# Kernel optimization log

Measured on AMD Instinct MI355X. Metric: run time of the kernel, lower is better.

The kernel has to match this reference:

```python
import jax, jax.numpy as jnp
import numpy as np

SCALING_FACTOR = 1.8
K = 10
ALPHA = 0.15
EPS = 1e-12


def setup_inputs() -> dict:
    key = jax.random.key(0)
    k1, k2, k3, k4 = jax.random.split(key, 4)
    N, E, IN, OUT = 100000, 3200000, 512, 256
    x = jax.random.normal(k1, (N, IN), dtype=jnp.float32)
    edge_index = jax.random.randint(k2, (2, E), 0, N, dtype=jnp.int64)
    W1 = jax.random.normal(k3, (OUT, IN), dtype=jnp.float32) * (1.0 / np.sqrt(IN))
    b1 = jax.random.normal(k4, (OUT,), dtype=jnp.float32) * 0.01
    return {"x": x, "edge_index": edge_index, "W1": W1, "b1": b1}


def _gcn_norm(edge_index, num_nodes):
    # add self-loops (PyG gcn_norm default), symmetric D^-1/2 (A+I) D^-1/2
    loops = jnp.arange(num_nodes, dtype=edge_index.dtype)
    src = jnp.concatenate([edge_index[0], loops])
    dst = jnp.concatenate([edge_index[1], loops])
    deg = jax.ops.segment_sum(jnp.ones_like(dst, dtype=jnp.float32), dst,
                              num_segments=num_nodes)
    dinv = jnp.where(deg > 0, jax.lax.rsqrt(deg), 0.0)
    norm = dinv[src] * dinv[dst]  # [E+N]
    return src, dst, norm


def reference(x, edge_index, W1, b1):
    N = x.shape[0]
    # linear1
    h = jnp.einsum('ni,oi->no', x, W1) + b1  # [N, OUT]
    # F.normalize(p=2, dim=1) * scaling_factor
    nrm = jnp.sqrt(jnp.sum(h * h, axis=1, keepdims=True))
    h = h / jnp.maximum(nrm, EPS) * SCALING_FACTOR
    # APPNP K=10, alpha=0.15
    src, dst, norm = _gcn_norm(edge_index, N)
    h0 = h

    def step(z, _):
        msg = z[src] * norm[:, None]                       # gather + scale
        agg = jax.ops.segment_sum(msg, dst, num_segments=N)  # scatter-add
        z = (1.0 - ALPHA) * agg + ALPHA * h0
        return z, None

    z, _ = jax.lax.scan(step, h, None, length=K)
    return z
```

## Files before the change

### kernel.cpp

```cpp
#include <hip/hip_runtime.h>
#include <hip/hip_fp16.h>


#define ALPHA 0.15f
#define BETA 0.85f
#define SCALE 1.8f

__global__ void transpose_w(const float* __restrict__ W1, float* __restrict__ Wt) {
    int i = blockIdx.x * blockDim.x + threadIdx.x;
    if (i >= 512 * 256) return;
    int k = i >> 8;
    int n = i & 255;
    Wt[i] = W1[n * 512 + k];
}

__global__ __launch_bounds__(256) void gemm_kernel(
    const float* __restrict__ A, const float* __restrict__ B,
    const float* __restrict__ bias, float* __restrict__ C, int M) {
    __shared__ float As[16][65];
    __shared__ float Bs[16][64];
    const int tid = threadIdx.x;
    const int tx = tid & 15;
    const int ty = tid >> 4;
    const int m0 = blockIdx.x * 64;
    const int n0 = blockIdx.y * 64;

    float acc[4][4];
#pragma unroll
    for (int i = 0; i < 4; i++)
#pragma unroll
        for (int j = 0; j < 4; j++) acc[i][j] = 0.0f;

    const int arow = tid >> 2;
    const int akseg = tid & 3;
    const int bkk = tid >> 4;
    const int bnseg = tid & 15;

    for (int k0 = 0; k0 < 512; k0 += 16) {
        float4 av = make_float4(0.f, 0.f, 0.f, 0.f);
        if (m0 + arow < M)
            av = *(const float4*)(A + (size_t)(m0 + arow) * 512 + k0 + akseg * 4);
        As[akseg * 4 + 0][arow] = av.x;
        As[akseg * 4 + 1][arow] = av.y;
        As[akseg * 4 + 2][arow] = av.z;
        As[akseg * 4 + 3][arow] = av.w;
        float4 bv = *(const float4*)(B + (size_t)(k0 + bkk) * 256 + n0 + bnseg * 4);
        *(float4*)(&Bs[bkk][bnseg * 4]) = bv;
        __syncthreads();

#pragma unroll
        for (int kk = 0; kk < 16; kk++) {
            float a[4], b[4];
#pragma unroll
            for (int i = 0; i < 4; i++) a[i] = As[kk][ty * 4 + i];
#pragma unroll
            for (int j = 0; j < 4; j++) b[j] = Bs[kk][tx * 4 + j];
#pragma unroll
            for (int i = 0; i < 4; i++)
#pragma unroll
                for (int j = 0; j < 4; j++) acc[i][j] += a[i] * b[j];
        }
        __syncthreads();
    }

    float4 bias4 = *(const float4*)(bias + n0 + tx * 4);
#pragma unroll
    for (int i = 0; i < 4; i++) {
        int m = m0 + ty * 4 + i;
        if (m < M) {
            float4 o;
            o.x = acc[i][0] + bias4.x;
            o.y = acc[i][1] + bias4.y;
            o.z = acc[i][2] + bias4.z;
            o.w = acc[i][3] + bias4.w;
            *(float4*)(C + (size_t)m * 256 + n0 + tx * 4) = o;
        }
    }
}

__global__ __launch_bounds__(256) void normalize_kernel(
    const float* __restrict__ h, const float* __restrict__ dinv,
    __half* __restrict__ h16, __half* __restrict__ y0, int N) {
    int n = blockIdx.x;
    if (n >= N) return;
    int t = threadIdx.x;
    float v = h[(size_t)n * 256 + t];
    float ss = v * v;
#pragma unroll
    for (int off = 32; off > 0; off >>= 1) ss += __shfl_down(ss, off, 64);
    __shared__ float wsum[4];
    int w = t >> 6, lane = t & 63;
    if (lane == 0) wsum[w] = ss;
    __syncthreads();
    float tot = wsum[0] + wsum[1] + wsum[2] + wsum[3];
    float nrm = sqrtf(tot);
    float s = SCALE / fmaxf(nrm, 1e-12f);
    float hv = v * s;
    h16[(size_t)n * 256 + t] = __float2half(hv);
    y0[(size_t)n * 256 + t] = __float2half(hv * dinv[n]);
}

__global__ void init_counts(int* __restrict__ counts, int N) {
    int i = blockIdx.x * blockDim.x + threadIdx.x;
    if (i < N) counts[i] = 1;
}

__global__ void count_kernel(const int* __restrict__ dst, int* __restrict__ counts, int E) {
    int i = blockIdx.x * blockDim.x + threadIdx.x;
    if (i < E) atomicAdd(&counts[dst[i]], 1);
}

__global__ void dinv_kernel(const int* __restrict__ counts, float* __restrict__ dinv, int N) {
    int i = blockIdx.x * blockDim.x + threadIdx.x;
    if (i < N) dinv[i] = rsqrtf((float)counts[i]);
}

__global__ __launch_bounds__(256) void scan_phase1(
    const int* __restrict__ counts, int* __restrict__ offsets,
    int* __restrict__ blocksums, int N) {
    __shared__ int sdata[256];
    int b = blockIdx.x;
    int base = b * 1024;
    int t = threadIdx.x;
    int v[4];
    int idx0 = base + t * 4;
    int sum = 0;
#pragma unroll
    for (int j = 0; j < 4; j++) {
        int i = idx0 + j;
        v[j] = (i < N) ? counts[i] : 0;
        sum += v[j];
    }
    sdata[t] = sum;
    __syncthreads();
    for (int off = 1; off < 256; off <<= 1) {
        int x = (t >= off) ? sdata[t - off] : 0;
        __syncthreads();
        sdata[t] += x;
        __syncthreads();
    }
    int incl = sdata[t];
    int excl = incl - sum;
    if (t == 255) blocksums[b] = incl;
    int run = excl;
#pragma unroll
    for (int j = 0; j < 4; j++) {
        int i = idx0 + j;
        if (i < N) offsets[i] = run;
        run += v[j];
    }
}

__global__ __launch_bounds__(128) void scan_phase2(int* __restrict__ blocksums, int nb) {
    __shared__ int s[128];
    int t = threadIdx.x;
    int v = (t < nb) ? blocksums[t] : 0;
    s[t] = v;
    __syncthreads();
    for (int off = 1; off < 128; off <<= 1) {
        int x = (t >= off) ? s[t - off] : 0;
        __syncthreads();
        s[t] += x;
        __syncthreads();
    }
    if (t < nb) blocksums[t] = s[t] - v;
}

__global__ void scan_phase3(int* __restrict__ offsets, const int* __restrict__ blocksums,
                            int* __restrict__ cursor, int N, int total) {
    int i = blockIdx.x * blockDim.x + threadIdx.x;
    if (i < N) {
        int o = offsets[i] + blocksums[i >> 10];
        offsets[i] = o;
        cursor[i] = o;
    }
    if (i == N) offsets[N] = total;
}

__global__ void fill_kernel(const int* __restrict__ src, const int* __restrict__ dst,
                            int* __restrict__ cursor, int* __restrict__ col, int E, int N) {
    int i = blockIdx.x * blockDim.x + threadIdx.x;
    int tot = E + N;
    if (i >= tot) return;
    int s, d;
    if (i < E) { s = src[i]; d = dst[i]; }
    else       { s = d = i - E; }
    int p = atomicAdd(&cursor[d], 1);
    col[p] = s;
}

__device__ __forceinline__ void acc_half4(float4& a, float2 r) {
    union { float2 f; __half2 h[2]; } u;
    u.f = r;
    float2 lo = __half22float2(u.h[0]);
    float2 hi = __half22float2(u.h[1]);
    a.x += lo.x; a.y += lo.y; a.z += hi.x; a.w += hi.y;
}

template <bool FINAL>
__global__ __launch_bounds__(256) void spmm_kernel(
    const __half* __restrict__ yin, const __half* __restrict__ h16,
    const int* __restrict__ offs, const int* __restrict__ col,
    const float* __restrict__ dinv, void* __restrict__ outp, int N) {
    int gw = blockIdx.x * 4 + (threadIdx.x >> 6);
    if (gw >= N) return;
    int lane = threadIdx.x & 63;
    int beg = offs[gw], end = offs[gw + 1];

    float4 a0 = make_float4(0.f, 0.f, 0.f, 0.f);
    float4 a1 = make_float4(0.f, 0.f, 0.f, 0.f);
    float4 a2 = make_float4(0.f, 0.f, 0.f, 0.f);
    float4 a3 = make_float4(0.f, 0.f, 0.f, 0.f);

    int e = beg;
    for (; e + 3 < end; e += 4) {
        int s0 = __builtin_nontemporal_load(col + e);
        int s1 = __builtin_nontemporal_load(col + e + 1);
        int s2 = __builtin_nontemporal_load(col + e + 2);
        int s3 = __builtin_nontemporal_load(col + e + 3);
        float2 r0 = ((const float2*)(yin + (size_t)s0 * 256))[lane];
        float2 r1 = ((const float2*)(yin + (size_t)s1 * 256))[lane];
        float2 r2 = ((const float2*)(yin + (size_t)s2 * 256))[lane];
        float2 r3 = ((const float2*)(yin + (size_t)s3 * 256))[lane];
        acc_half4(a0, r0); acc_half4(a1, r1); acc_half4(a2, r2); acc_half4(a3, r3);
    }
    for (; e < end; ++e) {
        int s0 = __builtin_nontemporal_load(col + e);
        float2 r0 = ((const float2*)(yin + (size_t)s0 * 256))[lane];
        acc_half4(a0, r0);
    }

    float dg = dinv[gw];
    float wd = BETA * dg;

    const float* hp = (const float*)(h16 + (size_t)gw * 256) + lane * 2;
    float hx = __builtin_nontemporal_load(hp);
    float hy = __builtin_nontemporal_load(hp + 1);
    float4 hh;
    {
        union { float f; __half2 h; } ux, uy;
        ux.f = hx; uy.f = hy;
        float2 lo = __half22float2(ux.h);
        float2 hi = __half22float2(uy.h);
        hh.x = lo.x; hh.y = lo.y; hh.z = hi.x; hh.w = hi.y;
    }

    float4 o;
    o.x = wd * (a0.x + a1.x + a2.x + a3.x) + ALPHA * hh.x;
    o.y = wd * (a0.y + a1.y + a2.y + a3.y) + ALPHA * hh.y;
    o.z = wd * (a0.z + a1.z + a2.z + a3.z) + ALPHA * hh.z;
    o.w = wd * (a0.w + a1.w + a2.w + a3.w) + ALPHA * hh.w;

    if (FINAL) {
        float* op = (float*)outp + (size_t)gw * 256 + lane * 4;
        __builtin_nontemporal_store(o.x, op);
        __builtin_nontemporal_store(o.y, op + 1);
        __builtin_nontemporal_store(o.z, op + 2);
        __builtin_nontemporal_store(o.w, op + 3);
    } else {
        __half2 p0 = __floats2half2_rn(o.x * dg, o.y * dg);
        __half2 p1 = __floats2half2_rn(o.z * dg, o.w * dg);
        union { float f; __half2 h; } u0, u1;
        u0.h = p0; u1.h = p1;
        float* op = (float*)((__half*)outp + (size_t)gw * 256) + lane * 2;
        __builtin_nontemporal_store(u0.f, op);
        __builtin_nontemporal_store(u1.f, op + 1);
    }
}

extern "C" void kernel_launch(void* const* d_in, const int* in_sizes, int n_in,
                              void* d_out, int out_size, void* d_ws, size_t ws_size,
                              hipStream_t stream) {
    const float* x  = (const float*)d_in[0];
    const int* ei   = (const int*)d_in[1];
    const float* W1 = (const float*)d_in[2];
    const float* b1 = (const float*)d_in[3];
    float* out = (float*)d_out;

    const int N = in_sizes[0] / 512;
    const int E = in_sizes[1] / 2;
    const int* src = ei;
    const int* dst = ei + E;
    const int NNZ = E + N;

    char* w = (char*)d_ws;
    float* h0 = (float*)w;      w += (size_t)N * 256 * 4;
    __half* h16 = (__half*)w;   w += (size_t)N * 256 * 2;
    __half* y0 = (__half*)w;    w += (size_t)N * 256 * 2;
    __half* yB = (__half*)w;    w += (size_t)N * 256 * 2;
    float* Wt = (float*)w;      w += (size_t)512 * 256 * 4;
    float* dinv = (float*)w;    w += (size_t)N * 4;
    int* counts = (int*)w;      w += (size_t)N * 4;
    int* offsets = (int*)w;     w += (size_t)(N + 64) * 4;
    int* blocksums = (int*)w;   w += 128 * 4;
    int* col = (int*)w;         w += (size_t)NNZ * 4;
    __half* yA = (__half*)h0;

    init_counts<<<(N + 255) / 256, 256, 0, stream>>>(counts, N);
    count_kernel<<<(E + 255) / 256, 256, 0, stream>>>(dst, counts, E);
    dinv_kernel<<<(N + 255) / 256, 256, 0, stream>>>(counts, dinv, N);
    transpose_w<<<(512 * 256 + 255) / 256, 256, 0, stream>>>(W1, Wt);
    dim3 ggrid((N + 63) / 64, 4);
    gemm_kernel<<<ggrid, 256, 0, stream>>>(x, Wt, b1, h0, N);
    normalize_kernel<<<N, 256, 0, stream>>>(h0, dinv, h16, y0, N);
    int nb = (N + 1023) / 1024;
    scan_phase1<<<nb, 256, 0, stream>>>(counts, offsets, blocksums, N);
    scan_phase2<<<1, 128, 0, stream>>>(blocksums, nb);
    scan_phase3<<<(N + 256) / 256, 256, 0, stream>>>(offsets, blocksums, counts, N, NNZ);
    fill_kernel<<<(NNZ + 255) / 256, 256, 0, stream>>>(src, dst, counts, col, E, N);
    int nblk = (N + 3) / 4;
    const __half* cur = y0;
    for (int it = 0; it < 9; ++it) {
        __half* nxt = (it & 1) ? yB : yA;
        spmm_kernel<false><<<nblk, 256, 0, stream>>>(cur, h16, offsets, col, dinv,
                                                     (void*)nxt, N);
        cur = nxt;
    }
    spmm_kernel<true><<<nblk, 256, 0, stream>>>(cur, h16, offsets, col, dinv,
                                                (void*)out, N);
}
```

Measured before the change: 3.473 ms.

## Replace FP32 SIMT GEMM with FP16 MFMA GEMM for linear layer

The scalar FP32 tiled GEMM is replaced by a kernel using 16x16x32 FP16 MFMA instructions. Each block covers 64 rows and all 256 output columns, with one wave per 64-column slab. Activations are converted to FP16 and staged in shared memory, while weights are pre-converted to FP16 and read directly from global memory. This targets the compute-bound linear layer, at the cost of lower input precision before normalization.

```diff
diff --git a/kernel.cpp b/kernel.cpp
--- a/kernel.cpp
+++ b/kernel.cpp
@@ -6,76 +6,100 @@
 #define BETA 0.85f
 #define SCALE 1.8f
 
-__global__ void transpose_w(const float* __restrict__ W1, float* __restrict__ Wt) {
-    int i = blockIdx.x * blockDim.x + threadIdx.x;
-    if (i >= 512 * 256) return;
-    int k = i >> 8;
-    int n = i & 255;
-    Wt[i] = W1[n * 512 + k];
-}
-
-__global__ __launch_bounds__(256) void gemm_kernel(
-    const float* __restrict__ A, const float* __restrict__ B,
+typedef _Float16 f16x8 __attribute__((ext_vector_type(8)));
+typedef float f32x4 __attribute__((ext_vector_type(4)));
+
+__global__ void convert_w(const float* __restrict__ W1, _Float16* __restrict__ Wh) {
+    int i = blockIdx.x * blockDim.x + threadIdx.x;
+    if (i < 256 * 512) Wh[i] = (_Float16)W1[i];
+}
+
+__global__ __launch_bounds__(256) void gemm_f16(
+    const float* __restrict__ A, const _Float16* __restrict__ Wh,
     const float* __restrict__ bias, float* __restrict__ C, int M) {
-    __shared__ float As[16][65];
-    __shared__ float Bs[16][64];
-    const int tid = threadIdx.x;
-    const int tx = tid & 15;
-    const int ty = tid >> 4;
-    const int m0 = blockIdx.x * 64;
-    const int n0 = blockIdx.y * 64;
-
-    float acc[4][4];
+    __shared__ _Float16 As[64][72];
+    const int tid  = threadIdx.x;
+    const int wv   = tid >> 6;
+    const int lane = tid & 63;
+    const int lc   = lane & 15;
+    const int lr   = lane >> 4;
+    const int m0   = blockIdx.x * 64;
+    const int n0w  = wv * 64;
+
+    f32x4 acc[4][4];
 #pragma unroll
     for (int i = 0; i < 4; i++)
 #pragma unroll
-        for (int j = 0; j < 4; j++) acc[i][j] = 0.0f;
-
-    const int arow = tid >> 2;
-    const int akseg = tid & 3;
-    const int bkk = tid >> 4;
-    const int bnseg = tid & 15;
-
-    for (int k0 = 0; k0 < 512; k0 += 16) {
-        float4 av = make_float4(0.f, 0.f, 0.f, 0.f);
-        if (m0 + arow < M)
-            av = *(const float4*)(A + (size_t)(m0 + arow) * 512 + k0 + akseg * 4);
-        As[akseg * 4 + 0][arow] = av.x;
-        As[akseg * 4 + 1][arow] = av.y;
-        As[akseg * 4 + 2][arow] = av.z;
-        As[akseg * 4 + 3][arow] = av.w;
-        float4 bv = *(const float4*)(B + (size_t)(k0 + bkk) * 256 + n0 + bnseg * 4);
-        *(float4*)(&Bs[bkk][bnseg * 4]) = bv;
-        __syncthreads();
-
-#pragma unroll
-        for (int kk = 0; kk < 16; kk++) {
-            float a[4], b[4];
-#pragma unroll
-            for (int i = 0; i < 4; i++) a[i] = As[kk][ty * 4 + i];
-#pragma unroll
-            for (int j = 0; j < 4; j++) b[j] = Bs[kk][tx * 4 + j];
-#pragma unroll
-            for (int i = 0; i < 4; i++)
-#pragma unroll
-                for (int j = 0; j < 4; j++) acc[i][j] += a[i] * b[j];
+        for (int j = 0; j < 4; j++) {
+            acc[i][j][0] = 0.f; acc[i][j][1] = 0.f;
+            acc[i][j][2] = 0.f; acc[i][j][3] = 0.f;
         }
-        __syncthreads();
-    }
-
-    float4 bias4 = *(const float4*)(bias + n0 + tx * 4);
-#pragma unroll
-    for (int i = 0; i < 4; i++) {
-        int m = m0 + ty * 4 + i;
-        if (m < M) {
-            float4 o;
-            o.x = acc[i][0] + bias4.x;
-            o.y = acc[i][1] + bias4.y;
-            o.z = acc[i][2] + bias4.z;
-            o.w = acc[i][3] + bias4.w;
-            *(float4*)(C + (size_t)m * 256 + n0 + tx * 4) = o;
+
+    const int srow = tid >> 2;
+    const int sseg = tid & 3;
+    const bool inb = (m0 + srow) < M;
+
+    for (int k0 = 0; k0 < 512; k0 += 64) {
+        float4 av0, av1, av2, av3;
+        if (inb) {
+            const float4* ap = (const float4*)(A + (size_t)(m0 + srow) * 512 + k0 + sseg * 16);
+            av0 = ap[0]; av1 = ap[1]; av2 = ap[2]; av3 = ap[3];
+        } else {
+            av0 = av1 = av2 = av3 = make_float4(0.f, 0.f, 0.f, 0.f);
         }
-    }
+        if (k0) __syncthreads();
+        f16x8 p0, p1;
+        p0[0] = (_Float16)av0.x; p0[1] = (_Float16)av0.y;
+        p0[2] = (_Float16)av0.z; p0[3] = (_Float16)av0.w;
+        p0[4] = (_Float16)av1.x; p0[5] = (_Float16)av1.y;
+        p0[6] = (_Float16)av1.z; p0[7] = (_Float16)av1.w;
+        p1[0] = (_Float16)av2.x; p1[1] = (_Float16)av2.y;
+        p1[2] = (_Float16)av2.z; p1[3] = (_Float16)av2.w;
+        p1[4] = (_Float16)av3.x; p1[5] = (_Float16)av3.y;
+        p1[6] = (_Float16)av3.z; p1[7] = (_Float16)av3.w;
+        _Float16* wp = &As[srow][sseg * 16];
+        *(f16x8*)wp = p0;
+        *(f16x8*)(wp + 8) = p1;
+        __syncthreads();
+
+        f16x8 bf[2][4];
+#pragma unroll
+        for (int s = 0; s < 2; ++s)
+#pragma unroll
+            for (int nt = 0; nt < 4; ++nt)
+                bf[s][nt] = *(const f16x8*)(Wh + (size_t)(n0w + nt * 16 + lc) * 512
+                                            + k0 + s * 32 + lr * 8);
+
+#pragma unroll
+        for (int s = 0; s < 2; ++s) {
+            f16x8 af[4];
+#pragma unroll
+            for (int mt = 0; mt < 4; ++mt)
+                af[mt] = *(const f16x8*)&As[mt * 16 + lc][s * 32 + lr * 8];
+#pragma unroll
+            for (int mt = 0; mt < 4; ++mt)
+#pragma unroll
+                for (int nt = 0; nt < 4; ++nt)
+                    acc[mt][nt] = __builtin_amdgcn_mfma_f32_16x16x32_f16(
+                        af[mt], bf[s][nt], acc[mt][nt], 0, 0, 0);
+        }
+    }
+
+    float bv[4];
+#pragma unroll
+    for (int nt = 0; nt < 4; ++nt) bv[nt] = bias[n0w + nt * 16 + lc];
+#pragma unroll
+    for (int mt = 0; mt < 4; ++mt)
+#pragma unroll
+        for (int r = 0; r < 4; ++r) {
+            int m = m0 + mt * 16 + lr * 4 + r;
+            if (m < M) {
+                float* cp = C + (size_t)m * 256 + n0w + lc;
+#pragma unroll
+                for (int nt = 0; nt < 4; ++nt)
+                    cp[nt * 16] = acc[mt][nt][r] + bv[nt];
+            }
+        }
 }
 
 __global__ __launch_bounds__(256) void normalize_kernel(
@@ -288,7 +312,7 @@
     __half* h16 = (__half*)w;   w += (size_t)N * 256 * 2;
     __half* y0 = (__half*)w;    w += (size_t)N * 256 * 2;
     __half* yB = (__half*)w;    w += (size_t)N * 256 * 2;
-    float* Wt = (float*)w;      w += (size_t)512 * 256 * 4;
+    _Float16* Wh = (_Float16*)w; w += (size_t)256 * 512 * 2;
     float* dinv = (float*)w;    w += (size_t)N * 4;
     int* counts = (int*)w;      w += (size_t)N * 4;
     int* offsets = (int*)w;     w += (size_t)(N + 64) * 4;
@@ -299,9 +323,8 @@
     init_counts<<<(N + 255) / 256, 256, 0, stream>>>(counts, N);
     count_kernel<<<(E + 255) / 256, 256, 0, stream>>>(dst, counts, E);
     dinv_kernel<<<(N + 255) / 256, 256, 0, stream>>>(counts, dinv, N);
-    transpose_w<<<(512 * 256 + 255) / 256, 256, 0, stream>>>(W1, Wt);
-    dim3 ggrid((N + 63) / 64, 4);
-    gemm_kernel<<<ggrid, 256, 0, stream>>>(x, Wt, b1, h0, N);
+    convert_w<<<(256 * 512 + 255) / 256, 256, 0, stream>>>(W1, Wh);
+    gemm_f16<<<(N + 63) / 64, 256, 0, stream>>>(x, Wh, b1, h0, N);
     normalize_kernel<<<N, 256, 0, stream>>>(h0, dinv, h16, y0, N);
     int nb = (N + 1023) / 1024;
     scan_phase1<<<nb, 256, 0, stream>>>(counts, offsets, blocksums, N);
```

Result: faster. 3.209 ms (-7.6%).
